# Kernel tuning notes

Measured on AMD Instinct MI355X. Metric: run time of the kernel, lower is better.

Reference implementation:

```python
import jax, jax.numpy as jnp
import numpy as np
from math import sqrt

B, S, E = 1, 2048, 1024
H, D = 16, 1024          # num_heads, d_model
DH = D // H              # head_dim = 64
EPS = 1e-5
LAMBDA_INIT = 0.8


def setup_inputs() -> dict:
    key = jax.random.key(0)
    ks = jax.random.split(key, 16)
    sd = 0.02
    x = jax.random.normal(ks[0], (B, S, E), dtype=jnp.float32)
    # causal mask: True => masked (matches torch masked_fill semantics)
    mask = jnp.triu(jnp.ones((S, S), dtype=bool), k=1)
    # per-head projection params stacked over heads: W [H, DH, E], b [H, DH]
    mk = lambda k: jax.random.normal(k, (H, DH, E), dtype=jnp.float32) * sd
    bk = lambda k: jax.random.normal(k, (H, DH), dtype=jnp.float32) * sd
    return {
        "x": x, "mask": mask,
        "Wq1": mk(ks[1]), "bq1": bk(ks[2]),
        "Wq2": mk(ks[3]), "bq2": bk(ks[4]),
        "Wk1": mk(ks[5]), "bk1": bk(ks[6]),
        "Wk2": mk(ks[7]), "bk2": bk(ks[8]),
        "Wv": mk(ks[9]), "bv": bk(ks[10]),
        "lam": jnp.full((H,), LAMBDA_INIT, dtype=jnp.float32),
        "gn_w": jnp.ones((D,), dtype=jnp.float32),
        "gn_b": jnp.zeros((D,), dtype=jnp.float32),
        "Wo": jax.random.normal(ks[11], (E, D), dtype=jnp.float32) * sd,
        "bo": jax.random.normal(ks[12], (E,), dtype=jnp.float32) * sd,
    }


def reference(x, mask, Wq1, bq1, Wq2, bq2, Wk1, bk1, Wk2, bk2, Wv, bv,
              lam, gn_w, gn_b, Wo, bo):
    scale = 1.0 / sqrt(DH)
    proj = lambda W, b: jnp.einsum('bse,hde->bhsd', x, W) + b[None, :, None, :]
    q1, q2 = proj(Wq1, bq1), proj(Wq2, bq2)
    k1, k2 = proj(Wk1, bk1), proj(Wk2, bk2)
    v = proj(Wv, bv)                                   # [B,H,S,DH]

    neg_inf = jnp.float32(-jnp.inf)
    s1 = jnp.einsum('bhsd,bhtd->bhst', q1, k1) * scale  # [B,H,S,S]
    s2 = jnp.einsum('bhsd,bhtd->bhst', q2, k2) * scale
    s1 = jnp.where(mask, neg_inf, s1)
    s2 = jnp.where(mask, neg_inf, s2)
    w = jax.nn.softmax(s1, axis=-1) - lam[None, :, None, None] * jax.nn.softmax(s2, axis=-1)
    # dropout is identity in eval mode
    out = jnp.einsum('bhst,bhtd->bhsd', w, v)           # [B,H,S,DH]

    # concat heads along feature dim -> [B,S,D]
    cat = out.transpose(0, 2, 1, 3).reshape(B, S, D)
    # GroupNorm over channels with num_groups=H: normalize each (DH, S) group
    xc = cat.transpose(0, 2, 1).reshape(B, H, DH, S)    # [B,H,DH,S]
    mu = xc.mean(axis=(2, 3), keepdims=True)
    var = xc.var(axis=(2, 3), keepdims=True)
    xn = ((xc - mu) * jax.lax.rsqrt(var + EPS)).reshape(B, D, S)
    xn = xn * gn_w[None, :, None] + gn_b[None, :, None]
    xn = xn.transpose(0, 2, 1)                          # [B,S,D]

    return xn @ Wo.T + bo                               # [B,S,E]
```

## Files before the change

kernel.cpp:

```cpp
#include <hip/hip_runtime.h>

#define S_LEN 2048
#define E_DIM 1024
#define NH 16
#define DHD 64
#define DMODEL 1024

typedef unsigned short u16;
typedef __attribute__((ext_vector_type(8))) short bf16x8;
typedef __attribute__((ext_vector_type(4))) float f32x4;

static constexpr float GN_EPS = 1e-5f;
static constexpr float QSCALE_LOG2E = 0.125f * 1.44269504088896340736f;

struct alignas(8) U16x4 { u16 x, y, z, w; };

__device__ __forceinline__ u16 f2bf(float f) {
    union { float f; unsigned u; } v; v.f = f;
    unsigned r = v.u + 0x7fffu + ((v.u >> 16) & 1u);
    return (u16)(r >> 16);
}
__device__ __forceinline__ u16 f2bf_trunc(float f) {
    union { float f; unsigned u; } v; v.f = f;
    return (u16)(v.u >> 16);
}
__device__ __forceinline__ float bf2f(u16 u) {
    union { unsigned u; float f; } v; v.u = ((unsigned)u) << 16; return v.f;
}

__device__ __forceinline__ f32x4 fzero() { f32x4 z = {0.f, 0.f, 0.f, 0.f}; return z; }

__device__ __forceinline__ void async16(const u16* g, u16* l) {
    __builtin_amdgcn_global_load_lds(
        (const __attribute__((address_space(1))) unsigned int*)g,
        (__attribute__((address_space(3))) unsigned int*)l, 16, 0, 0);
}

__device__ __forceinline__ void stage8(const u16* gbase, int gstride, u16* lds,
                                       int r0, int l) {
    const int cg = (l & 7) ^ (l >> 3);
    async16(gbase + (size_t)(r0 + (l >> 3)) * gstride + cg * 8, lds + r0 * 64);
}

__device__ __forceinline__ bf16x8 ldsfrag(const u16* lds, int r, int chunk) {
    return *(const bf16x8*)((const char*)lds + r * 128 + ((chunk ^ (r & 7)) << 4));
}

__global__ __launch_bounds__(256) void f2b_kernel(
    const float* __restrict__ x,
    const float* __restrict__ w0, const float* __restrict__ w1,
    const float* __restrict__ w2, const float* __restrict__ w3,
    const float* __restrict__ w4, const float* __restrict__ wo,
    u16* __restrict__ xb, u16* __restrict__ wall, u16* __restrict__ dwo)
{
    const int z = blockIdx.z;
    const float* src; u16* dst; int n;
    const int nw = NH * DHD * E_DIM;
    switch (z) {
        case 0: src = x;  dst = xb;            n = S_LEN * E_DIM;  break;
        case 1: src = w0; dst = wall;          n = nw; break;
        case 2: src = w1; dst = wall + nw;     n = nw; break;
        case 3: src = w2; dst = wall + 2 * nw; n = nw; break;
        case 4: src = w3; dst = wall + 3 * nw; n = nw; break;
        case 5: src = w4; dst = wall + 4 * nw; n = nw; break;
        default: src = wo; dst = dwo;          n = DMODEL * E_DIM; break;
    }
    int i = blockIdx.x * 256 + threadIdx.x;
    if (i * 4 < n) {
        float4 v = ((const float4*)src)[i];
        U16x4 o;
        o.x = f2bf(v.x); o.y = f2bf(v.y); o.z = f2bf(v.z); o.w = f2bf(v.w);
        ((U16x4*)dst)[i] = o;
    }
}

__global__ __launch_bounds__(256) void proj_mfma_kernel(
    const u16* __restrict__ xb, const u16* __restrict__ wall,
    const float* __restrict__ bq1, const float* __restrict__ bq2,
    const float* __restrict__ bk1, const float* __restrict__ bk2,
    const float* __restrict__ bv,
    u16* __restrict__ qk, u16* __restrict__ vt)
{
    __shared__ u16 As[128 * 64], Bs[128 * 64];
    const int m0 = blockIdx.x * 128, n0 = blockIdx.y * 128;
    const int t = threadIdx.x, w = t >> 6, l = t & 63;
    const int lane15 = l & 15, quad = l >> 4;
    const int wr = (w >> 1) * 64, wc = (w & 1) * 64;

    f32x4 acc[4][4];
    #pragma unroll
    for (int mi = 0; mi < 4; ++mi)
        #pragma unroll
        for (int ni = 0; ni < 4; ++ni) acc[mi][ni] = fzero();

    const u16* Ag = xb + (size_t)m0 * E_DIM;
    const u16* Bg = wall + (size_t)n0 * E_DIM;

    for (int k0 = 0; k0 < E_DIM; k0 += 64) {
        __syncthreads();
        #pragma unroll
        for (int i = 0; i < 4; ++i) stage8(Ag + k0, E_DIM, As, w * 32 + i * 8, l);
        #pragma unroll
        for (int i = 0; i < 4; ++i) stage8(Bg + k0, E_DIM, Bs, w * 32 + i * 8, l);
        __syncthreads();

        bf16x8 a[4][2], b[4][2];
        #pragma unroll
        for (int mi = 0; mi < 4; ++mi) {
            a[mi][0] = ldsfrag(As, wr + mi * 16 + lane15, quad);
            a[mi][1] = ldsfrag(As, wr + mi * 16 + lane15, 4 + quad);
        }
        #pragma unroll
        for (int ni = 0; ni < 4; ++ni) {
            b[ni][0] = ldsfrag(Bs, wc + ni * 16 + lane15, quad);
            b[ni][1] = ldsfrag(Bs, wc + ni * 16 + lane15, 4 + quad);
        }
        #pragma unroll
        for (int mi = 0; mi < 4; ++mi)
            #pragma unroll
            for (int ni = 0; ni < 4; ++ni) {
                acc[mi][ni] = __builtin_amdgcn_mfma_f32_16x16x32_bf16(
                    a[mi][0], b[ni][0], acc[mi][ni], 0, 0, 0);
                acc[mi][ni] = __builtin_amdgcn_mfma_f32_16x16x32_bf16(
                    a[mi][1], b[ni][1], acc[mi][ni], 0, 0, 0);
            }
    }

    const int tid = n0 >> 10;
    const float* bias = (tid == 0) ? bq1 : (tid == 1) ? bq2 :
                        (tid == 2) ? bk1 : (tid == 3) ? bk2 : bv;
    const float scl = (tid <= 1) ? QSCALE_LOG2E : 1.0f;
    const size_t nQKV = (size_t)NH * S_LEN * DHD;

    #pragma unroll
    for (int ni = 0; ni < 4; ++ni) {
        const int n = n0 + wc + ni * 16 + lane15;
        const int h = (n >> 6) & 15, d = n & 63;
        const float bb = bias[n & 1023];
        #pragma unroll
        for (int mi = 0; mi < 4; ++mi) {
            const int m = m0 + wr + mi * 16 + quad * 4;
            if (tid < 4) {
                u16* o = qk + tid * nQKV + ((size_t)h * S_LEN + m) * DHD + d;
                #pragma unroll
                for (int r = 0; r < 4; ++r)
                    o[r * DHD] = f2bf((acc[mi][ni][r] + bb) * scl);
            } else {
                U16x4 pk;
                pk.x = f2bf(acc[mi][ni][0] + bb);
                pk.y = f2bf(acc[mi][ni][1] + bb);
                pk.z = f2bf(acc[mi][ni][2] + bb);
                pk.w = f2bf(acc[mi][ni][3] + bb);
                *(U16x4*)(vt + ((size_t)h * DHD + d) * S_LEN + m) = pk;
            }
        }
    }
}

__global__ __launch_bounds__(256) void attn_mfma_kernel(
    const u16* __restrict__ qbase, const u16* __restrict__ kbase,
    const u16* __restrict__ vtb, u16* __restrict__ obase)
{
    __shared__ u16 Qs[64 * 64];
    __shared__ u16 Ks[2][64 * 64], Vs[2][64 * 64];
    __shared__ u16 Ps[4][16 * 64];
    const int z = blockIdx.z, h = blockIdx.y;
    const int qt = 31 - blockIdx.x;
    const int q0 = qt * 64;
    const size_t per = (size_t)NH * S_LEN * DHD;
    const u16* qg = qbase + z * per + (size_t)h * S_LEN * DHD;
    const u16* kg = kbase + z * per + (size_t)h * S_LEN * DHD;
    const u16* vg = vtb + (size_t)h * DHD * S_LEN;
    u16* og = obase + z * per + (size_t)h * S_LEN * DHD;
    const int t = threadIdx.x, w = t >> 6, l = t & 63;
    const int lane15 = l & 15, quad = l >> 4;
    u16* Pw = Ps[w];

    stage8(qg + (size_t)q0 * DHD, DHD, Qs, w * 16, l);
    stage8(qg + (size_t)q0 * DHD, DHD, Qs, w * 16 + 8, l);
    stage8(kg, DHD, Ks[0], w * 16, l);
    stage8(kg, DHD, Ks[0], w * 16 + 8, l);
    stage8(vg, S_LEN, Vs[0], w * 16, l);
    stage8(vg, S_LEN, Vs[0], w * 16 + 8, l);

    f32x4 O[4];
    float lsum[4];
    #pragma unroll
    for (int i = 0; i < 4; ++i) { O[i] = fzero(); lsum[i] = 0.f; }
    bf16x8 qa0, qa1;

    for (int kt = 0; kt <= qt; ++kt) {
        const int cur = kt & 1;
        __syncthreads();
        if (kt < qt) {
            const int t1 = (kt + 1) * 64;
            stage8(kg + (size_t)t1 * DHD, DHD, Ks[cur ^ 1], w * 16, l);
            stage8(kg + (size_t)t1 * DHD, DHD, Ks[cur ^ 1], w * 16 + 8, l);
            stage8(vg + t1, S_LEN, Vs[cur ^ 1], w * 16, l);
            stage8(vg + t1, S_LEN, Vs[cur ^ 1], w * 16 + 8, l);
        }
        if (kt == 0) {
            qa0 = ldsfrag(Qs, w * 16 + lane15, quad);
            qa1 = ldsfrag(Qs, w * 16 + lane15, 4 + quad);
        }

        f32x4 sc[4];
        #pragma unroll
        for (int nt = 0; nt < 4; ++nt) {
            sc[nt] = fzero();
            bf16x8 b0 = ldsfrag(Ks[cur], nt * 16 + lane15, quad);
            bf16x8 b1 = ldsfrag(Ks[cur], nt * 16 + lane15, 4 + quad);
            sc[nt] = __builtin_amdgcn_mfma_f32_16x16x32_bf16(qa0, b0, sc[nt], 0, 0, 0);
            sc[nt] = __builtin_amdgcn_mfma_f32_16x16x32_bf16(qa1, b1, sc[nt], 0, 0, 0);
        }

        const bool diag = (kt == qt);
        #pragma unroll
        for (int r = 0; r < 4; ++r) {
            const int lr = quad * 4 + r;
            const int qrl = w * 16 + lr;
            float p0 = __builtin_amdgcn_exp2f(sc[0][r]);
            float p1 = __builtin_amdgcn_exp2f(sc[1][r]);
            float p2 = __builtin_amdgcn_exp2f(sc[2][r]);
            float p3 = __builtin_amdgcn_exp2f(sc[3][r]);
            if (diag) {
                if (lane15      > qrl) p0 = 0.f;
                if (16 + lane15 > qrl) p1 = 0.f;
                if (32 + lane15 > qrl) p2 = 0.f;
                if (48 + lane15 > qrl) p3 = 0.f;
            }
            lsum[r] += (p0 + p1) + (p2 + p3);
            const int cb = (lane15 & 7) * 2;
            const int ch = lane15 >> 3;
            char* pb = (char*)Pw + lr * 128;
            *(u16*)(pb + (((0 + ch) ^ (lr & 7)) << 4) + cb) = f2bf_trunc(p0);
            *(u16*)(pb + (((2 + ch) ^ (lr & 7)) << 4) + cb) = f2bf_trunc(p1);
            *(u16*)(pb + (((4 + ch) ^ (lr & 7)) << 4) + cb) = f2bf_trunc(p2);
            *(u16*)(pb + (((6 + ch) ^ (lr & 7)) << 4) + cb) = f2bf_trunc(p3);
        }

        bf16x8 pa0 = ldsfrag(Pw, lane15, quad);
        bf16x8 pa1 = ldsfrag(Pw, lane15, 4 + quad);
        #pragma unroll
        for (int nt = 0; nt < 4; ++nt) {
            bf16x8 v0 = ldsfrag(Vs[cur], nt * 16 + lane15, quad);
            bf16x8 v1 = ldsfrag(Vs[cur], nt * 16 + lane15, 4 + quad);
            O[nt] = __builtin_amdgcn_mfma_f32_16x16x32_bf16(pa0, v0, O[nt], 0, 0, 0);
            O[nt] = __builtin_amdgcn_mfma_f32_16x16x32_bf16(pa1, v1, O[nt], 0, 0, 0);
        }
    }

    float inv[4];
    #pragma unroll
    for (int r = 0; r < 4; ++r) {
        float rs = lsum[r];
        rs += __shfl_xor(rs, 1);
        rs += __shfl_xor(rs, 2);
        rs += __shfl_xor(rs, 4);
        rs += __shfl_xor(rs, 8);
        inv[r] = 1.f / rs;
    }
    u16* orow = og + (size_t)(q0 + w * 16 + quad * 4) * DHD;
    #pragma unroll
    for (int nt = 0; nt < 4; ++nt) {
        const int d = nt * 16 + lane15;
        #pragma unroll
        for (int r = 0; r < 4; ++r)
            orow[r * DHD + d] = f2bf(O[nt][r] * inv[r]);
    }
}

__global__ __launch_bounds__(256) void gn_stats_kernel(
    const u16* __restrict__ o1, const u16* __restrict__ o2,
    const float* __restrict__ lam, float* __restrict__ part)
{
    const int h = blockIdx.x, p = blockIdx.y;
    const float vlam = lam[h];
    const int chunk = S_LEN * DHD / 8;
    const size_t base = (size_t)h * (S_LEN * DHD) + (size_t)p * chunk;
    const uint4* a = (const uint4*)(o1 + base);
    const uint4* b = (const uint4*)(o2 + base);
    float s = 0.f, ss = 0.f;
    for (int i = threadIdx.x; i < chunk / 8; i += 256) {
        uint4 av = a[i], bv = b[i];
        const unsigned aw[4] = {av.x, av.y, av.z, av.w};
        const unsigned bw[4] = {bv.x, bv.y, bv.z, bv.w};
        #pragma unroll
        for (int j = 0; j < 4; ++j) {
            union { unsigned u; float f; } lo_a, hi_a, lo_b, hi_b;
            lo_a.u = aw[j] << 16; hi_a.u = aw[j] & 0xffff0000u;
            lo_b.u = bw[j] << 16; hi_b.u = bw[j] & 0xffff0000u;
            float v0 = lo_a.f - vlam * lo_b.f;
            float v1 = hi_a.f - vlam * hi_b.f;
            s += v0 + v1;
            ss += v0 * v0 + v1 * v1;
        }
    }
    #pragma unroll
    for (int d = 1; d < 64; d <<= 1) { s += __shfl_xor(s, d); ss += __shfl_xor(ss, d); }
    __shared__ float red[8];
    const int w = threadIdx.x >> 6;
    if ((threadIdx.x & 63) == 0) { red[2 * w] = s; red[2 * w + 1] = ss; }
    __syncthreads();
    if (threadIdx.x == 0) {
        float S  = (red[0] + red[2]) + (red[4] + red[6]);
        float SS = (red[1] + red[3]) + (red[5] + red[7]);
        part[(blockIdx.x * 8 + p) * 2]     = S;
        part[(blockIdx.x * 8 + p) * 2 + 1] = SS;
    }
}

__global__ __launch_bounds__(256) void gn_apply_kernel(
    const u16* __restrict__ o1, const u16* __restrict__ o2,
    const float* __restrict__ lam, const float* __restrict__ part,
    const float* __restrict__ gw, const float* __restrict__ gb,
    u16* __restrict__ xnb)
{
    const int i4 = (blockIdx.x * 256 + threadIdx.x) * 4;
    const int dh = i4 & 63;
    const int s  = (i4 >> 6) & (S_LEN - 1);
    const int h  = i4 >> 17;
    const int d  = h * DHD + dh;
    float sum = 0.f, ssum = 0.f;
    #pragma unroll
    for (int p = 0; p < 8; ++p) {
        sum  += part[(h * 8 + p) * 2];
        ssum += part[(h * 8 + p) * 2 + 1];
    }
    const float n = (float)(S_LEN * DHD);
    const float mu = sum / n;
    const float rstd = rsqrtf(ssum / n - mu * mu + GN_EPS);
    const float vlam = lam[h];
    U16x4 a = *(const U16x4*)(o1 + i4);
    U16x4 b = *(const U16x4*)(o2 + i4);
    float4 g4 = *(const float4*)(gw + d);
    float4 b4 = *(const float4*)(gb + d);
    U16x4 o;
    o.x = f2bf((bf2f(a.x) - vlam * bf2f(b.x) - mu) * rstd * g4.x + b4.x);
    o.y = f2bf((bf2f(a.y) - vlam * bf2f(b.y) - mu) * rstd * g4.y + b4.y);
    o.z = f2bf((bf2f(a.z) - vlam * bf2f(b.z) - mu) * rstd * g4.z + b4.z);
    o.w = f2bf((bf2f(a.w) - vlam * bf2f(b.w) - mu) * rstd * g4.w + b4.w);
    *(U16x4*)(xnb + (size_t)s * DMODEL + d) = o;
}

__global__ __launch_bounds__(256) void out_mfma_kernel(
    const u16* __restrict__ xnb, const u16* __restrict__ wob,
    const float* __restrict__ bo, float* __restrict__ out)
{
    __shared__ u16 As[64 * 64], Bs[64 * 64];
    const int m0 = blockIdx.x * 64, n0 = blockIdx.y * 64;
    const int t = threadIdx.x, w = t >> 6, l = t & 63;
    const int lane15 = l & 15, quad = l >> 4;
    f32x4 acc[4];
    #pragma unroll
    for (int nt = 0; nt < 4; ++nt) acc[nt] = fzero();

    const u16* Ag = xnb + (size_t)m0 * DMODEL;
    const u16* Bg = wob + (size_t)n0 * DMODEL;
    for (int k0 = 0; k0 < DMODEL; k0 += 64) {
        __syncthreads();
        stage8(Ag + k0, DMODEL, As, w * 16, l);
        stage8(Ag + k0, DMODEL, As, w * 16 + 8, l);
        stage8(Bg + k0, DMODEL, Bs, w * 16, l);
        stage8(Bg + k0, DMODEL, Bs, w * 16 + 8, l);
        __syncthreads();
        bf16x8 a0 = ldsfrag(As, w * 16 + lane15, quad);
        bf16x8 a1 = ldsfrag(As, w * 16 + lane15, 4 + quad);
        #pragma unroll
        for (int nt = 0; nt < 4; ++nt) {
            bf16x8 b0 = ldsfrag(Bs, nt * 16 + lane15, quad);
            bf16x8 b1 = ldsfrag(Bs, nt * 16 + lane15, 4 + quad);
            acc[nt] = __builtin_amdgcn_mfma_f32_16x16x32_bf16(a0, b0, acc[nt], 0, 0, 0);
            acc[nt] = __builtin_amdgcn_mfma_f32_16x16x32_bf16(a1, b1, acc[nt], 0, 0, 0);
        }
    }
    #pragma unroll
    for (int nt = 0; nt < 4; ++nt) {
        const int n = n0 + nt * 16 + lane15;
        const float bb = bo[n];
        #pragma unroll
        for (int r = 0; r < 4; ++r)
            out[(size_t)(m0 + w * 16 + quad * 4 + r) * E_DIM + n] = acc[nt][r] + bb;
    }
}

extern "C" void kernel_launch(void* const* d_in, const int* in_sizes, int n_in,
                              void* d_out, int out_size, void* d_ws, size_t ws_size,
                              hipStream_t stream)
{
    const float* x   = (const float*)d_in[0];
    const float* Wq1 = (const float*)d_in[2];
    const float* bq1 = (const float*)d_in[3];
    const float* Wq2 = (const float*)d_in[4];
    const float* bq2 = (const float*)d_in[5];
    const float* Wk1 = (const float*)d_in[6];
    const float* bk1 = (const float*)d_in[7];
    const float* Wk2 = (const float*)d_in[8];
    const float* bk2 = (const float*)d_in[9];
    const float* Wv  = (const float*)d_in[10];
    const float* bv  = (const float*)d_in[11];
    const float* lam = (const float*)d_in[12];
    const float* gw  = (const float*)d_in[13];
    const float* gb  = (const float*)d_in[14];
    const float* Wo  = (const float*)d_in[15];
    const float* bo  = (const float*)d_in[16];
    float* out = (float*)d_out;

    char* p = (char*)d_ws;
    auto take = [&](size_t bytes) { char* r = p; p += (bytes + 255) & ~(size_t)255; return r; };
    const size_t nQKV = (size_t)NH * S_LEN * DHD;

    u16* xb   = (u16*)take(2 * (size_t)S_LEN * E_DIM);
    u16* wall = (u16*)take(2 * (size_t)5 * NH * DHD * E_DIM);
    u16* wob  = (u16*)take(2 * (size_t)DMODEL * E_DIM);
    u16* qk   = (u16*)take(2 * 4 * nQKV);
    u16* vtb  = (u16*)take(2 * nQKV);
    u16* o1   = (u16*)take(2 * 2 * nQKV);
    u16* xnb  = (u16*)take(2 * (size_t)S_LEN * DMODEL);
    float* part = (float*)take(4 * 256);

    f2b_kernel<<<dim3(2048, 1, 7), 256, 0, stream>>>(
        x, Wq1, Wq2, Wk1, Wk2, Wv, Wo, xb, wall, wob);

    proj_mfma_kernel<<<dim3(16, 40), 256, 0, stream>>>(
        xb, wall, bq1, bq2, bk1, bk2, bv, qk, vtb);

    attn_mfma_kernel<<<dim3(32, NH, 2), 256, 0, stream>>>(
        qk, qk + 2 * nQKV, vtb, o1);

    gn_stats_kernel<<<dim3(NH, 8), 256, 0, stream>>>(o1, o1 + nQKV, lam, part);
    gn_apply_kernel<<<dim3((int)(nQKV / 1024)), 256, 0, stream>>>(
        o1, o1 + nQKV, lam, part, gw, gb, xnb);

    out_mfma_kernel<<<dim3(32, 16), 256, 0, stream>>>(xnb, wob, bo, out);
}
```

Measured before the change: 249.7 us.

## Pair causal query tiles per block and triple-buffer K/V with manual waitcnt

Each attention block now processes two query tiles, bb and 31-bb, so every block does the same total causal work and the grid is halved. K/V staging moves from double to triple buffering with a prefetch distance of two, using explicit s_waitcnt vmcnt and s_barrier in place of __syncthreads. Q fragments are loaded straight from global memory into registers, dropping the Q shared tile. This targets the causal load imbalance and exposed load latency, but relies on stage8 issuing exactly the vmcnt counts assumed, and the smaller grid may lower occupancy.

```diff
diff --git a/kernel.cpp b/kernel.cpp
--- a/kernel.cpp
+++ b/kernel.cpp
@@ -161,12 +161,9 @@
     const u16* __restrict__ qbase, const u16* __restrict__ kbase,
     const u16* __restrict__ vtb, u16* __restrict__ obase)
 {
-    __shared__ u16 Qs[64 * 64];
-    __shared__ u16 Ks[2][64 * 64], Vs[2][64 * 64];
+    __shared__ u16 Ks[3][64 * 64], Vs[3][64 * 64];
     __shared__ u16 Ps[4][16 * 64];
-    const int z = blockIdx.z, h = blockIdx.y;
-    const int qt = 31 - blockIdx.x;
-    const int q0 = qt * 64;
+    const int z = blockIdx.z, h = blockIdx.y, bb = blockIdx.x;
     const size_t per = (size_t)NH * S_LEN * DHD;
     const u16* qg = qbase + z * per + (size_t)h * S_LEN * DHD;
     const u16* kg = kbase + z * per + (size_t)h * S_LEN * DHD;
@@ -176,97 +173,112 @@
     const int lane15 = l & 15, quad = l >> 4;
     u16* Pw = Ps[w];
 
-    stage8(qg + (size_t)q0 * DHD, DHD, Qs, w * 16, l);
-    stage8(qg + (size_t)q0 * DHD, DHD, Qs, w * 16 + 8, l);
-    stage8(kg, DHD, Ks[0], w * 16, l);
-    stage8(kg, DHD, Ks[0], w * 16 + 8, l);
-    stage8(vg, S_LEN, Vs[0], w * 16, l);
-    stage8(vg, S_LEN, Vs[0], w * 16 + 8, l);
-
-    f32x4 O[4];
-    float lsum[4];
-    #pragma unroll
-    for (int i = 0; i < 4; ++i) { O[i] = fzero(); lsum[i] = 0.f; }
-    bf16x8 qa0, qa1;
-
-    for (int kt = 0; kt <= qt; ++kt) {
-        const int cur = kt & 1;
+    for (int half = 0; half < 2; ++half) {
+        const int qt = half ? (31 - bb) : bb;
+        const int q0 = qt * 64;
+
+        const u16* qrow = qg + (size_t)(q0 + w * 16 + lane15) * DHD + quad * 8;
+        bf16x8 qa0 = *(const bf16x8*)(qrow);
+        bf16x8 qa1 = *(const bf16x8*)(qrow + 32);
+
+        stage8(kg, DHD, Ks[0], w * 16, l);
+        stage8(kg, DHD, Ks[0], w * 16 + 8, l);
+        stage8(vg, S_LEN, Vs[0], w * 16, l);
+        stage8(vg, S_LEN, Vs[0], w * 16 + 8, l);
+        if (qt >= 1) {
+            stage8(kg + (size_t)64 * DHD, DHD, Ks[1], w * 16, l);
+            stage8(kg + (size_t)64 * DHD, DHD, Ks[1], w * 16 + 8, l);
+            stage8(vg + 64, S_LEN, Vs[1], w * 16, l);
+            stage8(vg + 64, S_LEN, Vs[1], w * 16 + 8, l);
+        }
+
+        f32x4 O[4];
+        float lsum[4];
+        #pragma unroll
+        for (int i = 0; i < 4; ++i) { O[i] = fzero(); lsum[i] = 0.f; }
+
+        int cur = 0, pre = 2;
+        for (int kt = 0; kt <= qt; ++kt) {
+            if (kt < qt) asm volatile("s_waitcnt vmcnt(4)" ::: "memory");
+            else         asm volatile("s_waitcnt vmcnt(0)" ::: "memory");
+            asm volatile("s_barrier" ::: "memory");
+            if (kt + 2 <= qt) {
+                const int t2 = (kt + 2) * 64;
+                stage8(kg + (size_t)t2 * DHD, DHD, Ks[pre], w * 16, l);
+                stage8(kg + (size_t)t2 * DHD, DHD, Ks[pre], w * 16 + 8, l);
+                stage8(vg + t2, S_LEN, Vs[pre], w * 16, l);
+                stage8(vg + t2, S_LEN, Vs[pre], w * 16 + 8, l);
+            }
+            const u16* Kc = Ks[cur];
+            const u16* Vc = Vs[cur];
+
+            f32x4 sc[4];
+            #pragma unroll
+            for (int nt = 0; nt < 4; ++nt) {
+                sc[nt] = fzero();
+                bf16x8 b0 = ldsfrag(Kc, nt * 16 + lane15, quad);
+                bf16x8 b1 = ldsfrag(Kc, nt * 16 + lane15, 4 + quad);
+                sc[nt] = __builtin_amdgcn_mfma_f32_16x16x32_bf16(qa0, b0, sc[nt], 0, 0, 0);
+                sc[nt] = __builtin_amdgcn_mfma_f32_16x16x32_bf16(qa1, b1, sc[nt], 0, 0, 0);
+            }
+
+            const bool diag = (kt == qt);
+            #pragma unroll
+            for (int r = 0; r < 4; ++r) {
+                const int lr = quad * 4 + r;
+                const int qrl = w * 16 + lr;
+                float p0 = __builtin_amdgcn_exp2f(sc[0][r]);
+                float p1 = __builtin_amdgcn_exp2f(sc[1][r]);
+                float p2 = __builtin_amdgcn_exp2f(sc[2][r]);
+                float p3 = __builtin_amdgcn_exp2f(sc[3][r]);
+                if (diag) {
+                    if (lane15      > qrl) p0 = 0.f;
+                    if (16 + lane15 > qrl) p1 = 0.f;
+                    if (32 + lane15 > qrl) p2 = 0.f;
+                    if (48 + lane15 > qrl) p3 = 0.f;
+                }
+                lsum[r] += (p0 + p1) + (p2 + p3);
+                const int cb = (lane15 & 7) * 2;
+                const int ch = lane15 >> 3;
+                char* pb = (char*)Pw + lr * 128;
+                *(u16*)(pb + (((0 + ch) ^ (lr & 7)) << 4) + cb) = f2bf_trunc(p0);
+                *(u16*)(pb + (((2 + ch) ^ (lr & 7)) << 4) + cb) = f2bf_trunc(p1);
+                *(u16*)(pb + (((4 + ch) ^ (lr & 7)) << 4) + cb) = f2bf_trunc(p2);
+                *(u16*)(pb + (((6 + ch) ^ (lr & 7)) << 4) + cb) = f2bf_trunc(p3);
+            }
+
+            bf16x8 pa0 = ldsfrag(Pw, lane15, quad);
+            bf16x8 pa1 = ldsfrag(Pw, lane15, 4 + quad);
+            #pragma unroll
+            for (int nt = 0; nt < 4; ++nt) {
+                bf16x8 v0 = ldsfrag(Vc, nt * 16 + lane15, quad);
+                bf16x8 v1 = ldsfrag(Vc, nt * 16 + lane15, 4 + quad);
+                O[nt] = __builtin_amdgcn_mfma_f32_16x16x32_bf16(pa0, v0, O[nt], 0, 0, 0);
+                O[nt] = __builtin_amdgcn_mfma_f32_16x16x32_bf16(pa1, v1, O[nt], 0, 0, 0);
+            }
+            cur = (cur == 2) ? 0 : cur + 1;
+            pre = (pre == 2) ? 0 : pre + 1;
+        }
+
+        float inv[4];
+        #pragma unroll
+        for (int r = 0; r < 4; ++r) {
+            float rs = lsum[r];
+            rs += __shfl_xor(rs, 1);
+            rs += __shfl_xor(rs, 2);
+            rs += __shfl_xor(rs, 4);
+            rs += __shfl_xor(rs, 8);
+            inv[r] = 1.f / rs;
+        }
+        u16* orow = og + (size_t)(q0 + w * 16 + quad * 4) * DHD;
+        #pragma unroll
+        for (int nt = 0; nt < 4; ++nt) {
+            const int d = nt * 16 + lane15;
+            #pragma unroll
+            for (int r = 0; r < 4; ++r)
+                orow[r * DHD + d] = f2bf(O[nt][r] * inv[r]);
+        }
         __syncthreads();
-        if (kt < qt) {
-            const int t1 = (kt + 1) * 64;
-            stage8(kg + (size_t)t1 * DHD, DHD, Ks[cur ^ 1], w * 16, l);
-            stage8(kg + (size_t)t1 * DHD, DHD, Ks[cur ^ 1], w * 16 + 8, l);
-            stage8(vg + t1, S_LEN, Vs[cur ^ 1], w * 16, l);
-            stage8(vg + t1, S_LEN, Vs[cur ^ 1], w * 16 + 8, l);
-        }
-        if (kt == 0) {
-            qa0 = ldsfrag(Qs, w * 16 + lane15, quad);
-            qa1 = ldsfrag(Qs, w * 16 + lane15, 4 + quad);
-        }
-
-        f32x4 sc[4];
-        #pragma unroll
-        for (int nt = 0; nt < 4; ++nt) {
-            sc[nt] = fzero();
-            bf16x8 b0 = ldsfrag(Ks[cur], nt * 16 + lane15, quad);
-            bf16x8 b1 = ldsfrag(Ks[cur], nt * 16 + lane15, 4 + quad);
-            sc[nt] = __builtin_amdgcn_mfma_f32_16x16x32_bf16(qa0, b0, sc[nt], 0, 0, 0);
-            sc[nt] = __builtin_amdgcn_mfma_f32_16x16x32_bf16(qa1, b1, sc[nt], 0, 0, 0);
-        }
-
-        const bool diag = (kt == qt);
-        #pragma unroll
-        for (int r = 0; r < 4; ++r) {
-            const int lr = quad * 4 + r;
-            const int qrl = w * 16 + lr;
-            float p0 = __builtin_amdgcn_exp2f(sc[0][r]);
-            float p1 = __builtin_amdgcn_exp2f(sc[1][r]);
-            float p2 = __builtin_amdgcn_exp2f(sc[2][r]);
-            float p3 = __builtin_amdgcn_exp2f(sc[3][r]);
-            if (diag) {
-                if (lane15      > qrl) p0 = 0.f;
-                if (16 + lane15 > qrl) p1 = 0.f;
-                if (32 + lane15 > qrl) p2 = 0.f;
-                if (48 + lane15 > qrl) p3 = 0.f;
-            }
-            lsum[r] += (p0 + p1) + (p2 + p3);
-            const int cb = (lane15 & 7) * 2;
-            const int ch = lane15 >> 3;
-            char* pb = (char*)Pw + lr * 128;
-            *(u16*)(pb + (((0 + ch) ^ (lr & 7)) << 4) + cb) = f2bf_trunc(p0);
-            *(u16*)(pb + (((2 + ch) ^ (lr & 7)) << 4) + cb) = f2bf_trunc(p1);
-            *(u16*)(pb + (((4 + ch) ^ (lr & 7)) << 4) + cb) = f2bf_trunc(p2);
-            *(u16*)(pb + (((6 + ch) ^ (lr & 7)) << 4) + cb) = f2bf_trunc(p3);
-        }
-
-        bf16x8 pa0 = ldsfrag(Pw, lane15, quad);
-        bf16x8 pa1 = ldsfrag(Pw, lane15, 4 + quad);
-        #pragma unroll
-        for (int nt = 0; nt < 4; ++nt) {
-            bf16x8 v0 = ldsfrag(Vs[cur], nt * 16 + lane15, quad);
-            bf16x8 v1 = ldsfrag(Vs[cur], nt * 16 + lane15, 4 + quad);
-            O[nt] = __builtin_amdgcn_mfma_f32_16x16x32_bf16(pa0, v0, O[nt], 0, 0, 0);
-            O[nt] = __builtin_amdgcn_mfma_f32_16x16x32_bf16(pa1, v1, O[nt], 0, 0, 0);
-        }
-    }
-
-    float inv[4];
-    #pragma unroll
-    for (int r = 0; r < 4; ++r) {
-        float rs = lsum[r];
-        rs += __shfl_xor(rs, 1);
-        rs += __shfl_xor(rs, 2);
-        rs += __shfl_xor(rs, 4);
-        rs += __shfl_xor(rs, 8);
-        inv[r] = 1.f / rs;
-    }
-    u16* orow = og + (size_t)(q0 + w * 16 + quad * 4) * DHD;
-    #pragma unroll
-    for (int nt = 0; nt < 4; ++nt) {
-        const int d = nt * 16 + lane15;
-        #pragma unroll
-        for (int r = 0; r < 4; ++r)
-            orow[r * DHD + d] = f2bf(O[nt][r] * inv[r]);
     }
 }
 
@@ -425,7 +437,7 @@
     proj_mfma_kernel<<<dim3(16, 40), 256, 0, stream>>>(
         xb, wall, bq1, bq2, bk1, bk2, bv, qk, vtb);
 
-    attn_mfma_kernel<<<dim3(32, NH, 2), 256, 0, stream>>>(
+    attn_mfma_kernel<<<dim3(16, NH, 2), 256, 0, stream>>>(
         qk, qk + 2 * nQKV, vtb, o1);
 
     gn_stats_kernel<<<dim3(NH, 8), 256, 0, stream>>>(o1, o1 + nQKV, lam, part);
```

New measurement: 219.5 us. -12.1%, faster.
